# Optimization experiments

Hardware: AMD Instinct MI355X
Metric: run time of the kernel (lower is better)

Reference implementation:

```python
import jax, jax.numpy as jnp
import numpy as np

N = 30000
E = 480000
C_IN, H = 16, 4
NEG_SLOPE = 0.2  # PyG GATv2Conv default negative_slope


def gatv2(x, src, dst, Wl, bl, Wr, br, att, bias, heads, outc, concat, n):
    # PyG GATv2Conv (share_weights=False): e_ij = att . leaky_relu(Wl x_j + Wr x_i)
    xl = (x @ Wl + bl).reshape(n, heads, outc)   # source transform
    xr = (x @ Wr + br).reshape(n, heads, outc)   # target transform
    e = jax.nn.leaky_relu(xl[src] + xr[dst], NEG_SLOPE)        # [E,H,C]
    logits = jnp.einsum('ehc,hc->eh', e, att)                  # [E,H]
    m = jax.lax.stop_gradient(jax.ops.segment_max(logits, dst, num_segments=n))
    ex = jnp.exp(logits - m[dst])
    denom = jax.ops.segment_sum(ex, dst, num_segments=n)
    alpha = ex / denom[dst]                                    # scatter-softmax over in-edges
    out = jax.ops.segment_sum(alpha[:, :, None] * xl[src], dst, num_segments=n)  # [N,H,C]
    out = out.reshape(n, heads * outc) if concat else out.mean(axis=1)
    return out + bias


def setup_inputs() -> dict:
    key = jax.random.key(0)
    ks = jax.random.split(key, 16)
    s = 0.05
    inp = {
        'x': jax.random.uniform(ks[0], (N, C_IN), dtype=jnp.float32),
        'edge_index': jax.random.randint(ks[1], (2, E), 0, N, dtype=jnp.int32),
        'lower_bound': jnp.zeros((C_IN,), jnp.float32),
        'upper_bound': jnp.ones((C_IN,), jnp.float32),
        # Layer 1: GATv2Conv(16 -> 32 per head, heads=4, concat=True) => 128
        'W1l': jax.random.normal(ks[2], (C_IN, H * 32), jnp.float32) * s,
        'b1l': jnp.zeros((H * 32,), jnp.float32),
        'W1r': jax.random.normal(ks[3], (C_IN, H * 32), jnp.float32) * s,
        'b1r': jnp.zeros((H * 32,), jnp.float32),
        'att1': jax.random.normal(ks[4], (H, 32), jnp.float32) * s,
        'bias1': jnp.zeros((H * 32,), jnp.float32),
        # Layer 2: GATv2Conv(128 -> 64 per head, heads=4, concat=False) => 64
        'W2l': jax.random.normal(ks[5], (128, H * 64), jnp.float32) * s,
        'b2l': jnp.zeros((H * 64,), jnp.float32),
        'W2r': jax.random.normal(ks[6], (128, H * 64), jnp.float32) * s,
        'b2r': jnp.zeros((H * 64,), jnp.float32),
        'att2': jax.random.normal(ks[7], (H, 64), jnp.float32) * s,
        'bias2': jnp.zeros((64,), jnp.float32),
        # Final linear head 64 -> 5
        'W3': jax.random.normal(ks[8], (64, 5), jnp.float32) * s,
        'b3': jnp.zeros((5,), jnp.float32),
    }
    return inp


def reference(x, edge_index, lower_bound, upper_bound,
              W1l, b1l, W1r, b1r, att1, bias1,
              W2l, b2l, W2r, b2r, att2, bias2,
              W3, b3):
    n = x.shape[0]
    # min-max normalization
    y = (x - lower_bound) / (upper_bound - lower_bound)
    # add self loops (PyG GATv2Conv default add_self_loops=True)
    loops = jnp.tile(jnp.arange(n, dtype=edge_index.dtype)[None, :], (2, 1))
    ei = jnp.concatenate([edge_index, loops], axis=1)
    src, dst = ei[0], ei[1]
    y = gatv2(y, src, dst, W1l, b1l, W1r, b1r, att1, bias1, H, 32, True, n)
    y = jax.nn.relu(y)
    y = gatv2(y, src, dst, W2l, b2l, W2r, b2r, att2, bias2, H, 64, False, n)
    y = jax.nn.relu(y)
    y = y @ W3 + b3
    return jax.nn.sigmoid(y)
```

## Files before the change

kernel.cpp:

```cpp
#include <hip/hip_runtime.h>

#define H 4
#define D1 128
#define D2 256
#define CIN 16
#define SLOPE 0.2f
#define LOG2E 1.4426950408889634f

typedef short short8v __attribute__((ext_vector_type(8)));
typedef float float4v __attribute__((ext_vector_type(4)));
typedef float float2v __attribute__((ext_vector_type(2)));
typedef __fp16 half2v __attribute__((ext_vector_type(2)));

__device__ __forceinline__ unsigned short f2bf(float f) {
    unsigned int u = __float_as_uint(f);
    u += 0x7FFFu + ((u >> 16) & 1u);
    return (unsigned short)(u >> 16);
}
__device__ __forceinline__ half2v pkrtz(float a, float b) {
    return __builtin_amdgcn_cvt_pkrtz(a, b);
}
__device__ __forceinline__ half2v h2_from_u32(unsigned u) {
    return __builtin_bit_cast(half2v, u);
}
__device__ __forceinline__ unsigned u32_from_h2(half2v h) {
    return __builtin_bit_cast(unsigned, h);
}
__device__ __forceinline__ unsigned short f2fp8x2(float a, float b) {
    return (unsigned short)__builtin_amdgcn_cvt_pk_fp8_f32(a, b, 0, false);
}
template<bool HI>
__device__ __forceinline__ half2v fp8x2_to_h2(unsigned u) {
#if __has_builtin(__builtin_amdgcn_cvt_scalef32_pk_f16_fp8)
    return __builtin_amdgcn_cvt_scalef32_pk_f16_fp8(u, 1.f, HI);
#else
    float2v f = __builtin_amdgcn_cvt_pk_f32_fp8(u, HI);
    return pkrtz(f.x, f.y);
#endif
}
__device__ __forceinline__ float fdot2(half2v a, half2v b, float c) {
#if __has_builtin(__builtin_amdgcn_fdot2)
    return __builtin_amdgcn_fdot2(a, b, c, false);
#else
    return c + (float)a.x * (float)b.x + (float)a.y * (float)b.y;
#endif
}
__device__ __forceinline__ int rfl(int v) {
    return __builtin_amdgcn_readfirstlane(v);
}

__device__ __forceinline__ float dpp_sum16(float x) {
    float t;
    t = __int_as_float(__builtin_amdgcn_mov_dpp(__float_as_int(x), 0xB1, 0xF, 0xF, true));
    x += t;
    t = __int_as_float(__builtin_amdgcn_mov_dpp(__float_as_int(x), 0x4E, 0xF, 0xF, true));
    x += t;
    t = __int_as_float(__builtin_amdgcn_mov_dpp(__float_as_int(x), 0x141, 0xF, 0xF, true));
    x += t;
    t = __int_as_float(__builtin_amdgcn_mov_dpp(__float_as_int(x), 0x140, 0xF, 0xF, true));
    x += t;
    return x;
}

__global__ void k_hist(const int* __restrict__ ei, int E, int ET,
                       int* __restrict__ deg) {
    int idx = blockIdx.x * blockDim.x + threadIdx.x;
    if (idx >= ET) return;
    int dst = (idx < E) ? ei[E + idx] : idx - E;
    atomicAdd(&deg[dst], 1);
}

__global__ __launch_bounds__(1024) void k_scan_one(
        const int* __restrict__ deg, int* __restrict__ rp,
        int* __restrict__ cur, int* __restrict__ ord, int n) {
    __shared__ int wsum[16];
    __shared__ int dh[256];
    int t = threadIdx.x;
    int lane = t & 63, w = t >> 6;
    if (t < 256) dh[t] = 0;
    int base = t * 32;
    int vals[32];
    const int4* dp = (const int4*)deg;
#pragma unroll
    for (int q = 0; q < 8; ++q) {
        int4 v = dp[(base >> 2) + q];
        vals[4 * q + 0] = v.x; vals[4 * q + 1] = v.y;
        vals[4 * q + 2] = v.z; vals[4 * q + 3] = v.w;
    }
    int loc[32];
    int s = 0;
#pragma unroll
    for (int k = 0; k < 32; ++k) {
        int idx = base + k;
        int v = (idx < n) ? vals[k] : 0;
        loc[k] = s;
        s += v;
    }
    int inc = s;
#pragma unroll
    for (int off = 1; off < 64; off <<= 1) {
        int u = __shfl_up(inc, off, 64);
        if (lane >= off) inc += u;
    }
    int excl = inc - s;
    if (lane == 63) wsum[w] = inc;
    __syncthreads();
    if (w == 0) {
        int v = (lane < 16) ? wsum[lane] : 0;
        int winc = v;
#pragma unroll
        for (int off = 1; off < 16; off <<= 1) {
            int u = __shfl_up(winc, off, 64);
            if (lane >= off) winc += u;
        }
        if (lane < 16) wsum[lane] = winc - v;
    }
    __syncthreads();
    int offw = wsum[w] + excl;
#pragma unroll
    for (int q = 0; q < 8; ++q) {
        int i0 = base + 4 * q;
        if (i0 + 3 < n) {
            *(int4*)(rp + i0) = make_int4(offw + loc[4 * q + 0], offw + loc[4 * q + 1],
                                          offw + loc[4 * q + 2], offw + loc[4 * q + 3]);
            *(int4*)(cur + i0) = make_int4(0, 0, 0, 0);
        } else {
#pragma unroll
            for (int e = 0; e < 4; ++e) {
                int idx = i0 + e;
                if (idx < n) { rp[idx] = offw + loc[4 * q + e]; cur[idx] = 0; }
            }
        }
    }
#pragma unroll
    for (int k = 0; k < 32; ++k) {
        int idx = base + k;
        if (idx < n) {
            int bin = 255 - min(vals[k], 255);
            atomicAdd(&dh[bin], 1);
        }
    }
    __syncthreads();
    if (t < 64) {
        int b0 = dh[4 * t], b1 = dh[4 * t + 1], b2 = dh[4 * t + 2], b3 = dh[4 * t + 3];
        int s4 = b0 + b1 + b2 + b3;
        int inc2 = s4;
#pragma unroll
        for (int off = 1; off < 64; off <<= 1) {
            int u = __shfl_up(inc2, off, 64);
            if (lane >= off) inc2 += u;
        }
        int ex = inc2 - s4;
        dh[4 * t] = ex; dh[4 * t + 1] = ex + b0;
        dh[4 * t + 2] = ex + b0 + b1; dh[4 * t + 3] = ex + b0 + b1 + b2;
    }
    __syncthreads();
#pragma unroll
    for (int k = 0; k < 32; ++k) {
        int idx = base + k;
        if (idx < n) {
            int bin = 255 - min(vals[k], 255);
            int pos = atomicAdd(&dh[bin], 1);
            ord[pos] = idx;
        }
    }
}

__global__ void k_fill(const int* __restrict__ ei, int E, int ET,
                       const int* __restrict__ rp, int* __restrict__ cur,
                       int* __restrict__ eord) {
    int idx = blockIdx.x * blockDim.x + threadIdx.x;
    if (idx >= ET) return;
    int src, dst;
    if (idx < E) { src = ei[idx]; dst = ei[E + idx]; }
    else         { src = dst = idx - E; }
    int pos = atomicAdd(&cur[dst], 1);
    eord[rp[dst] + pos] = src;
}

__global__ __launch_bounds__(256) void k_prep(
        const float* __restrict__ x, const float* __restrict__ lb,
        const float* __restrict__ ub,
        const float* __restrict__ Wl, const float* __restrict__ bl,
        const float* __restrict__ Wr, const float* __restrict__ br,
        unsigned char* __restrict__ xl8, unsigned short* __restrict__ xr16,
        const float* __restrict__ W2l, const float* __restrict__ W2r,
        unsigned short* __restrict__ W2t,
        int* __restrict__ deg, int n, int B1) {
    __shared__ float Wls[CIN][D1];
    __shared__ float Wrs[CIN][D1];
    __shared__ float ys[16][CIN];
    int b = blockIdx.x;
    int t = threadIdx.x;
    if (b >= B1) {
        int rb = b - B1;
        if (rb < 256) {
            int idx = rb * 256 + t;
            int k = idx >> 9, c = idx & 511;
            float v = (c < 256) ? W2l[k * 256 + c] : W2r[k * 256 + (c - 256)];
            W2t[(size_t)c * 128 + k] = f2bf(v);
        } else {
            int idx = (rb - 256) * 256 + t;
            if (idx < n) deg[idx] = 0;
        }
        return;
    }
    int i0 = b * 16;
#pragma unroll
    for (int i = 0; i < 8; ++i) {
        int flat = t + 256 * i;
        int k = flat >> 7, c = flat & 127;
        Wls[k][c] = Wl[k * D1 + c];
        Wrs[k][c] = Wr[k * D1 + c];
    }
    {
        int node = t >> 4, k = t & 15;
        int gi = i0 + node;
        float xv = (gi < n) ? x[(size_t)gi * CIN + k] : 0.f;
        ys[node][k] = (xv - lb[k]) / (ub[k] - lb[k]);
    }
    __syncthreads();
    int c = t & 127;
    bool left = t < 128;
    const float (*Ws)[D1] = left ? Wls : Wrs;
    float bias = left ? bl[c] : br[c];
    for (int j = 0; j < 16; ++j) {
        float acc = bias;
#pragma unroll
        for (int k = 0; k < CIN; ++k) acc += ys[j][k] * Ws[k][c];
        int gi = i0 + j;
        float other = __shfl_xor(acc, 1);
        if (gi < n && !(c & 1)) {
            if (left)
                *(unsigned short*)(xl8 + (size_t)gi * D1 + c) = f2fp8x2(acc, other);
            else
                *(unsigned*)(xr16 + (size_t)gi * D1 + c) = u32_from_h2(pkrtz(acc, other));
        }
    }
}

__global__ __launch_bounds__(256) void k_lin2_mfma(
        const unsigned short* __restrict__ h1b,
        const unsigned short* __restrict__ W2t,
        const float* __restrict__ b2l, const float* __restrict__ b2r,
        unsigned char* __restrict__ xl2,
        unsigned short* __restrict__ xr2,
        int n) {
    __shared__ unsigned short At[128 * 128];
    __shared__ unsigned short Bt[128 * 128];
    int t = threadIdx.x;
    int row0 = blockIdx.x * 128;
    int col0 = blockIdx.y * 128;

    {
        int r = t >> 1, hh = (t & 1) * 64;
        bool ok = (row0 + r) < n;
        const unsigned short* gA = h1b + (size_t)(row0 + r) * 128 + hh;
        const unsigned short* gB = W2t + (size_t)(col0 + r) * 128 + hh;
#pragma unroll
        for (int i = 0; i < 8; ++i) {
            uint4 vA = ok ? *(const uint4*)(gA + i * 8) : make_uint4(0, 0, 0, 0);
            uint4 vB = *(const uint4*)(gB + i * 8);
            int col = hh + i * 8;
            int idx = (r * 128 + col) ^ ((r & 15) << 3);
            *(uint4*)&At[idx] = vA;
            *(uint4*)&Bt[idx] = vB;
        }
    }
    __syncthreads();

    int w = t >> 6, l = t & 63;
    int wr = w >> 1, wc = w & 1;
    float4v acc[4][4];
#pragma unroll
    for (int m = 0; m < 4; ++m)
#pragma unroll
        for (int nn = 0; nn < 4; ++nn) acc[m][nn] = (float4v)0.f;

#pragma unroll
    for (int ks = 0; ks < 4; ++ks) {
        int kb = ks * 32 + ((l >> 4) << 3);
        short8v a[4], b[4];
#pragma unroll
        for (int m = 0; m < 4; ++m) {
            int r = wr * 64 + m * 16 + (l & 15);
            a[m] = *(const short8v*)&At[(r * 128 + kb) ^ ((r & 15) << 3)];
        }
#pragma unroll
        for (int nn = 0; nn < 4; ++nn) {
            int c = wc * 64 + nn * 16 + (l & 15);
            b[nn] = *(const short8v*)&Bt[(c * 128 + kb) ^ ((c & 15) << 3)];
        }
#pragma unroll
        for (int m = 0; m < 4; ++m)
#pragma unroll
            for (int nn = 0; nn < 4; ++nn)
                acc[m][nn] = __builtin_amdgcn_mfma_f32_16x16x32_bf16(
                    a[m], b[nn], acc[m][nn], 0, 0, 0);
    }

    if (col0 < 256) {
        const float* bp = b2l;
        int cb = col0;
#pragma unroll
        for (int nn = 0; nn < 4; ++nn) {
            int colc = cb + wc * 64 + nn * 16 + (l & 15);
            float bv = bp[colc];
#pragma unroll
            for (int m = 0; m < 4; ++m) {
                int rbase = row0 + wr * 64 + m * 16 + ((l >> 4) << 2);
#pragma unroll
                for (int r = 0; r < 4; ++r) {
                    int row = rbase + r;
                    float val = acc[m][nn][r] + bv;
                    float other = __shfl_xor(val, 1);
                    if (!(l & 1) && row < n)
                        *(unsigned short*)(xl2 + (size_t)row * 256 + colc) =
                            f2fp8x2(val, other);
                }
            }
        }
    } else {
        const float* bp = b2r;
        int cb = col0 - 256;
#pragma unroll
        for (int nn = 0; nn < 4; ++nn) {
            int colc = cb + wc * 64 + nn * 16 + (l & 15);
            float bv = bp[colc];
#pragma unroll
            for (int m = 0; m < 4; ++m) {
                int rbase = row0 + wr * 64 + m * 16 + ((l >> 4) << 2);
#pragma unroll
                for (int r = 0; r < 4; ++r) {
                    int row = rbase + r;
                    float val = acc[m][nn][r] + bv;
                    float other = __shfl_xor(val, 1);
                    if (!(l & 1) && row < n)
                        *(unsigned*)(xr2 + (size_t)row * 256 + colc) =
                            u32_from_h2(pkrtz(val, other));
                }
            }
        }
    }
}

__global__ __launch_bounds__(256) void k_agg1(
        const unsigned char* __restrict__ xl8, const unsigned short* __restrict__ xr16,
        const float* __restrict__ att, const float* __restrict__ bias,
        const int* __restrict__ rp, const int* __restrict__ deg,
        const int* __restrict__ eord, const int* __restrict__ ord,
        unsigned short* __restrict__ h1b, int n) {
    int t = threadIdx.x;
    int node0 = blockIdx.x * 4 + (t >> 6);
    int l = t & 63;
    bool valid = node0 < n;
    int node = rfl(ord[valid ? node0 : n - 1]);
    half2v xr01 = h2_from_u32(((const unsigned*)xr16)[(size_t)node * 64 + l]);
    float2 av = *(const float2*)(att + 2 * l);
    half2v av01 = pkrtz(av.x * LOG2E, av.y * LOG2E);
    half2v slp = pkrtz(SLOPE, SLOPE);
    int start = rfl(rp[node]);
    int cnt   = valid ? deg[node] : 0;
    cnt = rfl(cnt);
    const unsigned short* xlp = (const unsigned short*)xl8;
    float d = 0.f;
    half2v a01 = pkrtz(0.f, 0.f);
    int cnt4 = cnt & ~3;
    unsigned g0, g1, g2, g3;
    int s0, s1, s2, s3;
    if (cnt4 > 0) {
        int4 iv = *(const int4*)(eord + start);
        s0 = rfl(iv.x); s1 = rfl(iv.y); s2 = rfl(iv.z); s3 = rfl(iv.w);
        g0 = xlp[(unsigned)(s0 << 6) + l]; g1 = xlp[(unsigned)(s1 << 6) + l];
        g2 = xlp[(unsigned)(s2 << 6) + l]; g3 = xlp[(unsigned)(s3 << 6) + l];
    }
    for (int j = 0; j < cnt4; j += 4) {
        unsigned c0 = g0, c1 = g1, c2 = g2, c3 = g3;
        int jn = j + 4;
        if (jn < cnt4) {
            int4 iv = *(const int4*)(eord + start + jn);
            s0 = rfl(iv.x); s1 = rfl(iv.y); s2 = rfl(iv.z); s3 = rfl(iv.w);
            g0 = xlp[(unsigned)(s0 << 6) + l]; g1 = xlp[(unsigned)(s1 << 6) + l];
            g2 = xlp[(unsigned)(s2 << 6) + l]; g3 = xlp[(unsigned)(s3 << 6) + l];
        }
        half2v x0 = fp8x2_to_h2<false>(c0), x1 = fp8x2_to_h2<false>(c1);
        half2v x2 = fp8x2_to_h2<false>(c2), x3 = fp8x2_to_h2<false>(c3);
        half2v s;
        float lg0, lg1, lg2, lg3;
        s = x0 + xr01; s = __builtin_elementwise_max(s, s * slp); lg0 = fdot2(av01, s, 0.f);
        s = x1 + xr01; s = __builtin_elementwise_max(s, s * slp); lg1 = fdot2(av01, s, 0.f);
        s = x2 + xr01; s = __builtin_elementwise_max(s, s * slp); lg2 = fdot2(av01, s, 0.f);
        s = x3 + xr01; s = __builtin_elementwise_max(s, s * slp); lg3 = fdot2(av01, s, 0.f);
        lg0 = dpp_sum16(lg0); lg1 = dpp_sum16(lg1);
        lg2 = dpp_sum16(lg2); lg3 = dpp_sum16(lg3);
        float e0 = exp2f(lg0), e1 = exp2f(lg1);
        float e2 = exp2f(lg2), e3 = exp2f(lg3);
        d += (e0 + e1) + (e2 + e3);
        a01 += pkrtz(e0, e0) * x0;
        a01 += pkrtz(e1, e1) * x1;
        a01 += pkrtz(e2, e2) * x2;
        a01 += pkrtz(e3, e3) * x3;
    }
    for (int j = cnt4; j < cnt; ++j) {
        int sj = rfl(eord[start + j]);
        half2v x0 = fp8x2_to_h2<false>((unsigned)xlp[(unsigned)(sj << 6) + l]);
        half2v s0v = x0 + xr01;
        s0v = __builtin_elementwise_max(s0v, s0v * slp);
        float lg0 = fdot2(av01, s0v, 0.f);
        lg0 = dpp_sum16(lg0);
        float e0 = exp2f(lg0);
        d += e0;
        a01 += pkrtz(e0, e0) * x0;
    }
    if (valid) {
        float inv = 1.f / d;
        float o0 = fmaxf((float)a01.x * inv + bias[2 * l + 0], 0.f);
        float o1 = fmaxf((float)a01.y * inv + bias[2 * l + 1], 0.f);
        ((unsigned*)h1b)[(size_t)node * 64 + l] =
            ((unsigned)f2bf(o1) << 16) | f2bf(o0);
    }
}

__global__ __launch_bounds__(256) void k_agg2(
        const unsigned char* __restrict__ xl8, const unsigned short* __restrict__ xr16,
        const float* __restrict__ att, const float* __restrict__ b2,
        const float* __restrict__ W3, const float* __restrict__ b3,
        const int* __restrict__ rp, const int* __restrict__ deg,
        const int* __restrict__ eord, const int* __restrict__ ord,
        float* __restrict__ out, int n) {
    int t = threadIdx.x;
    int node0 = blockIdx.x * 4 + (t >> 6);
    int l = t & 63;
    bool valid = node0 < n;
    int node = rfl(ord[valid ? node0 : n - 1]);
    uint2 xru = ((const uint2*)xr16)[(size_t)node * 64 + l];
    half2v xr01 = h2_from_u32(xru.x), xr23 = h2_from_u32(xru.y);
    float4 av = *(const float4*)(att + 4 * l);
    half2v av01 = pkrtz(av.x * LOG2E, av.y * LOG2E);
    half2v av23 = pkrtz(av.z * LOG2E, av.w * LOG2E);
    half2v slp = pkrtz(SLOPE, SLOPE);
    int start = rfl(rp[node]);
    int cnt   = valid ? deg[node] : 0;
    cnt = rfl(cnt);
    const unsigned* xlp = (const unsigned*)xl8;
    float d = 0.f;
    half2v a01 = pkrtz(0.f, 0.f), a23 = pkrtz(0.f, 0.f);
    int cnt4 = cnt & ~3;
    unsigned g0, g1, g2, g3;
    int s0, s1, s2, s3;
    if (cnt4 > 0) {
        int4 iv = *(const int4*)(eord + start);
        s0 = rfl(iv.x); s1 = rfl(iv.y); s2 = rfl(iv.z); s3 = rfl(iv.w);
        g0 = xlp[(unsigned)(s0 << 6) + l]; g1 = xlp[(unsigned)(s1 << 6) + l];
        g2 = xlp[(unsigned)(s2 << 6) + l]; g3 = xlp[(unsigned)(s3 << 6) + l];
    }
    for (int j = 0; j < cnt4; j += 4) {
        unsigned c0 = g0, c1 = g1, c2 = g2, c3 = g3;
        int jn = j + 4;
        if (jn < cnt4) {
            int4 iv = *(const int4*)(eord + start + jn);
            s0 = rfl(iv.x); s1 = rfl(iv.y); s2 = rfl(iv.z); s3 = rfl(iv.w);
            g0 = xlp[(unsigned)(s0 << 6) + l]; g1 = xlp[(unsigned)(s1 << 6) + l];
            g2 = xlp[(unsigned)(s2 << 6) + l]; g3 = xlp[(unsigned)(s3 << 6) + l];
        }
        half2v x0lo = fp8x2_to_h2<false>(c0), x0hi = fp8x2_to_h2<true>(c0);
        half2v x1lo = fp8x2_to_h2<false>(c1), x1hi = fp8x2_to_h2<true>(c1);
        half2v x2lo = fp8x2_to_h2<false>(c2), x2hi = fp8x2_to_h2<true>(c2);
        half2v x3lo = fp8x2_to_h2<false>(c3), x3hi = fp8x2_to_h2<true>(c3);
        half2v s;
        float lg0, lg1, lg2, lg3;
        s = x0lo + xr01; s = __builtin_elementwise_max(s, s * slp); lg0 = fdot2(av01, s, 0.f);
        s = x0hi + xr23; s = __builtin_elementwise_max(s, s * slp); lg0 = fdot2(av23, s, lg0);
        s = x1lo + xr01; s = __builtin_elementwise_max(s, s * slp); lg1 = fdot2(av01, s, 0.f);
        s = x1hi + xr23; s = __builtin_elementwise_max(s, s * slp); lg1 = fdot2(av23, s, lg1);
        s = x2lo + xr01; s = __builtin_elementwise_max(s, s * slp); lg2 = fdot2(av01, s, 0.f);
        s = x2hi + xr23; s = __builtin_elementwise_max(s, s * slp); lg2 = fdot2(av23, s, lg2);
        s = x3lo + xr01; s = __builtin_elementwise_max(s, s * slp); lg3 = fdot2(av01, s, 0.f);
        s = x3hi + xr23; s = __builtin_elementwise_max(s, s * slp); lg3 = fdot2(av23, s, lg3);
        lg0 = dpp_sum16(lg0); lg1 = dpp_sum16(lg1);
        lg2 = dpp_sum16(lg2); lg3 = dpp_sum16(lg3);
        float e0 = exp2f(lg0), e1 = exp2f(lg1);
        float e2 = exp2f(lg2), e3 = exp2f(lg3);
        d += (e0 + e1) + (e2 + e3);
        half2v ep;
        ep = pkrtz(e0, e0); a01 += ep * x0lo; a23 += ep * x0hi;
        ep = pkrtz(e1, e1); a01 += ep * x1lo; a23 += ep * x1hi;
        ep = pkrtz(e2, e2); a01 += ep * x2lo; a23 += ep * x2hi;
        ep = pkrtz(e3, e3); a01 += ep * x3lo; a23 += ep * x3hi;
    }
    for (int j = cnt4; j < cnt; ++j) {
        int sj = rfl(eord[start + j]);
        unsigned p0 = xlp[(unsigned)(sj << 6) + l];
        half2v xlo = fp8x2_to_h2<false>(p0), xhi = fp8x2_to_h2<true>(p0);
        half2v s;
        float lg0;
        s = xlo + xr01; s = __builtin_elementwise_max(s, s * slp); lg0 = fdot2(av01, s, 0.f);
        s = xhi + xr23; s = __builtin_elementwise_max(s, s * slp); lg0 = fdot2(av23, s, lg0);
        lg0 = dpp_sum16(lg0);
        float e0 = exp2f(lg0);
        d += e0;
        half2v ep = pkrtz(e0, e0);
        a01 += ep * xlo; a23 += ep * xhi;
    }
    float inv = 1.f / d;
    float v0 = (float)a01.x * inv, v1 = (float)a01.y * inv;
    float v2 = (float)a23.x * inv, v3 = (float)a23.y * inv;
    v0 += __shfl_xor(v0, 16); v1 += __shfl_xor(v1, 16);
    v2 += __shfl_xor(v2, 16); v3 += __shfl_xor(v3, 16);
    v0 += __shfl_xor(v0, 32); v1 += __shfl_xor(v1, 32);
    v2 += __shfl_xor(v2, 32); v3 += __shfl_xor(v3, 32);
    int c0i = 4 * (l & 15);
    v0 = fmaxf(0.25f * v0 + b2[c0i + 0], 0.f);
    v1 = fmaxf(0.25f * v1 + b2[c0i + 1], 0.f);
    v2 = fmaxf(0.25f * v2 + b2[c0i + 2], 0.f);
    v3 = fmaxf(0.25f * v3 + b2[c0i + 3], 0.f);
    float p0, p1, p2, p3, p4;
    {
        const float* w0 = W3 + (c0i + 0) * 5;
        const float* w1 = W3 + (c0i + 1) * 5;
        const float* w2 = W3 + (c0i + 2) * 5;
        const float* w3 = W3 + (c0i + 3) * 5;
        p0 = v0 * w0[0] + v1 * w1[0] + v2 * w2[0] + v3 * w3[0];
        p1 = v0 * w0[1] + v1 * w1[1] + v2 * w2[1] + v3 * w3[1];
        p2 = v0 * w0[2] + v1 * w1[2] + v2 * w2[2] + v3 * w3[2];
        p3 = v0 * w0[3] + v1 * w1[3] + v2 * w2[3] + v3 * w3[3];
        p4 = v0 * w0[4] + v1 * w1[4] + v2 * w2[4] + v3 * w3[4];
    }
    p0 = dpp_sum16(p0); p1 = dpp_sum16(p1); p2 = dpp_sum16(p2);
    p3 = dpp_sum16(p3); p4 = dpp_sum16(p4);
    if (l == 0 && valid) {
        float* o = out + (size_t)node * 5;
        o[0] = 1.f / (1.f + __expf(-(p0 + b3[0])));
        o[1] = 1.f / (1.f + __expf(-(p1 + b3[1])));
        o[2] = 1.f / (1.f + __expf(-(p2 + b3[2])));
        o[3] = 1.f / (1.f + __expf(-(p3 + b3[3])));
        o[4] = 1.f / (1.f + __expf(-(p4 + b3[4])));
    }
}

extern "C" void kernel_launch(void* const* d_in, const int* in_sizes, int n_in,
                              void* d_out, int out_size, void* d_ws, size_t ws_size,
                              hipStream_t stream) {
    const float* x     = (const float*)d_in[0];
    const int*   ei    = (const int*)d_in[1];
    const float* lb    = (const float*)d_in[2];
    const float* ub    = (const float*)d_in[3];
    const float* W1l   = (const float*)d_in[4];
    const float* b1l   = (const float*)d_in[5];
    const float* W1r   = (const float*)d_in[6];
    const float* b1r   = (const float*)d_in[7];
    const float* att1  = (const float*)d_in[8];
    const float* bias1 = (const float*)d_in[9];
    const float* W2l   = (const float*)d_in[10];
    const float* b2l   = (const float*)d_in[11];
    const float* W2r   = (const float*)d_in[12];
    const float* b2r   = (const float*)d_in[13];
    const float* att2  = (const float*)d_in[14];
    const float* bias2 = (const float*)d_in[15];
    const float* W3    = (const float*)d_in[16];
    const float* b3    = (const float*)d_in[17];

    int n  = in_sizes[0] / CIN;
    int E  = in_sizes[1] / 2;
    int ET = E + n;

    char* ws = (char*)d_ws;
    size_t off = 0;
    auto alloc = [&](size_t nbytes) {
        void* p = ws + off;
        off += (nbytes + 255) & ~(size_t)255;
        return p;
    };
    unsigned char*  xl1 = (unsigned char*)alloc((size_t)n * D1);
    unsigned short* xr1 = (unsigned short*)alloc((size_t)n * D1 * 2);
    unsigned short* h1b = (unsigned short*)alloc((size_t)n * D1 * 2);
    unsigned char*  xl2 = (unsigned char*)alloc((size_t)n * D2);
    unsigned short* xr2 = (unsigned short*)alloc((size_t)n * D2 * 2);
    unsigned short* W2t = (unsigned short*)alloc((size_t)512 * 128 * 2);
    int* deg  = (int*)alloc((size_t)n * 4 + 8192);
    int* cur  = (int*)alloc((size_t)n * 4);
    int* rp   = (int*)alloc((size_t)n * 4);
    int* ord  = (int*)alloc((size_t)n * 4);
    int* eord = (int*)alloc((size_t)ET * 4 + 256);

    int B1 = (n + 15) / 16;
    int BZ = (n + 255) / 256;
    k_prep<<<B1 + 256 + BZ, 256, 0, stream>>>(
        x, lb, ub, W1l, b1l, W1r, b1r, xl1, xr1, W2l, W2r, W2t, deg, n, B1);

    k_hist<<<(ET + 255) / 256, 256, 0, stream>>>(ei, E, ET, deg);
    k_scan_one<<<1, 1024, 0, stream>>>(deg, rp, cur, ord, n);
    k_fill<<<(ET + 255) / 256, 256, 0, stream>>>(ei, E, ET, rp, cur, eord);

    k_agg1<<<(n + 3) / 4, 256, 0, stream>>>(xl1, xr1, att1, bias1, rp, deg,
                                            eord, ord, h1b, n);

    dim3 g2((n + 127) / 128, 4);
    k_lin2_mfma<<<g2, 256, 0, stream>>>(h1b, W2t, b2l, b2r, xl2, xr2, n);
    k_agg2<<<(n + 3) / 4, 256, 0, stream>>>(xl2, xr2, att2, bias2, W3, b3,
                                            rp, deg, eord, ord, (float*)d_out, n);
}
```

Baseline: 170.5 us.

## Process four edges per wave concurrently with 16 lanes per edge row

Both aggregation kernels now assign each 16-lane group of a wave to a different edge, so every lane loads a wide vector of the fp8 source row instead of a 2 or 4 byte slice. The per-edge logit reduction shrinks to a 4-lane DPP sum, which matches per-head grouping. Partial accumulators are combined across the four groups with xor shuffles at the end. Remainder edges are handled by masking instead of a scalar tail loop. This aims to cut the number of loop iterations and cross-lane reductions per edge, at the cost of divergent per-lane gather addresses, extra end-of-loop shuffles, and fp16 accumulation being split and re-summed.

```diff
diff --git a/kernel.cpp b/kernel.cpp
--- a/kernel.cpp
+++ b/kernel.cpp
@@ -48,18 +48,19 @@
 __device__ __forceinline__ int rfl(int v) {
     return __builtin_amdgcn_readfirstlane(v);
 }
-
-__device__ __forceinline__ float dpp_sum16(float x) {
+__device__ __forceinline__ float dpp_sum4(float x) {
     float t;
     t = __int_as_float(__builtin_amdgcn_mov_dpp(__float_as_int(x), 0xB1, 0xF, 0xF, true));
     x += t;
     t = __int_as_float(__builtin_amdgcn_mov_dpp(__float_as_int(x), 0x4E, 0xF, 0xF, true));
     x += t;
-    t = __int_as_float(__builtin_amdgcn_mov_dpp(__float_as_int(x), 0x141, 0xF, 0xF, true));
-    x += t;
-    t = __int_as_float(__builtin_amdgcn_mov_dpp(__float_as_int(x), 0x140, 0xF, 0xF, true));
-    x += t;
     return x;
+}
+template<int XOR>
+__device__ __forceinline__ half2v h2_xor_add(half2v v) {
+    unsigned u = u32_from_h2(v);
+    unsigned o = (unsigned)__shfl_xor((int)u, XOR);
+    return v + h2_from_u32(o);
 }
 
 __global__ void k_hist(const int* __restrict__ ei, int E, int ET,
@@ -352,72 +353,77 @@
         unsigned short* __restrict__ h1b, int n) {
     int t = threadIdx.x;
     int node0 = blockIdx.x * 4 + (t >> 6);
-    int l = t & 63;
+    int l = t & 63, g = l >> 4, p = l & 15;
     bool valid = node0 < n;
     int node = rfl(ord[valid ? node0 : n - 1]);
-    half2v xr01 = h2_from_u32(((const unsigned*)xr16)[(size_t)node * 64 + l]);
-    float2 av = *(const float2*)(att + 2 * l);
-    half2v av01 = pkrtz(av.x * LOG2E, av.y * LOG2E);
+    uint4 xq = *(const uint4*)(xr16 + (size_t)node * 128 + p * 8);
+    half2v xr0 = h2_from_u32(xq.x), xr1 = h2_from_u32(xq.y);
+    half2v xr2_ = h2_from_u32(xq.z), xr3 = h2_from_u32(xq.w);
+    const float4* avp = (const float4*)(att + p * 8);
+    float4 af0 = avp[0], af1 = avp[1];
+    half2v av0 = pkrtz(af0.x * LOG2E, af0.y * LOG2E);
+    half2v av1 = pkrtz(af0.z * LOG2E, af0.w * LOG2E);
+    half2v av2 = pkrtz(af1.x * LOG2E, af1.y * LOG2E);
+    half2v av3 = pkrtz(af1.z * LOG2E, af1.w * LOG2E);
     half2v slp = pkrtz(SLOPE, SLOPE);
     int start = rfl(rp[node]);
-    int cnt   = valid ? deg[node] : 0;
+    int cnt = valid ? deg[node] : 0;
     cnt = rfl(cnt);
-    const unsigned short* xlp = (const unsigned short*)xl8;
     float d = 0.f;
-    half2v a01 = pkrtz(0.f, 0.f);
-    int cnt4 = cnt & ~3;
-    unsigned g0, g1, g2, g3;
-    int s0, s1, s2, s3;
-    if (cnt4 > 0) {
-        int4 iv = *(const int4*)(eord + start);
-        s0 = rfl(iv.x); s1 = rfl(iv.y); s2 = rfl(iv.z); s3 = rfl(iv.w);
-        g0 = xlp[(unsigned)(s0 << 6) + l]; g1 = xlp[(unsigned)(s1 << 6) + l];
-        g2 = xlp[(unsigned)(s2 << 6) + l]; g3 = xlp[(unsigned)(s3 << 6) + l];
-    }
-    for (int j = 0; j < cnt4; j += 4) {
-        unsigned c0 = g0, c1 = g1, c2 = g2, c3 = g3;
+    half2v a0 = pkrtz(0.f, 0.f), a1 = a0, a2 = a0, a3 = a0;
+    int cntR = (cnt + 3) & ~3;
+    int ecl = cnt - 1;
+    uint2 row;
+    if (cntR > 0) {
+        int src = eord[start + min(g, ecl)];
+        row = *(const uint2*)(xl8 + ((unsigned)src << 7) + p * 8);
+    }
+    for (int j = 0; j < cntR; j += 4) {
+        uint2 cr = row;
+        bool live = (j + g) <= ecl;
         int jn = j + 4;
-        if (jn < cnt4) {
-            int4 iv = *(const int4*)(eord + start + jn);
-            s0 = rfl(iv.x); s1 = rfl(iv.y); s2 = rfl(iv.z); s3 = rfl(iv.w);
-            g0 = xlp[(unsigned)(s0 << 6) + l]; g1 = xlp[(unsigned)(s1 << 6) + l];
-            g2 = xlp[(unsigned)(s2 << 6) + l]; g3 = xlp[(unsigned)(s3 << 6) + l];
-        }
-        half2v x0 = fp8x2_to_h2<false>(c0), x1 = fp8x2_to_h2<false>(c1);
-        half2v x2 = fp8x2_to_h2<false>(c2), x3 = fp8x2_to_h2<false>(c3);
+        if (jn < cntR) {
+            int src = eord[start + min(jn + g, ecl)];
+            row = *(const uint2*)(xl8 + ((unsigned)src << 7) + p * 8);
+        }
+        half2v x0 = fp8x2_to_h2<false>(cr.x), x1 = fp8x2_to_h2<true>(cr.x);
+        half2v x2 = fp8x2_to_h2<false>(cr.y), x3 = fp8x2_to_h2<true>(cr.y);
         half2v s;
-        float lg0, lg1, lg2, lg3;
-        s = x0 + xr01; s = __builtin_elementwise_max(s, s * slp); lg0 = fdot2(av01, s, 0.f);
-        s = x1 + xr01; s = __builtin_elementwise_max(s, s * slp); lg1 = fdot2(av01, s, 0.f);
-        s = x2 + xr01; s = __builtin_elementwise_max(s, s * slp); lg2 = fdot2(av01, s, 0.f);
-        s = x3 + xr01; s = __builtin_elementwise_max(s, s * slp); lg3 = fdot2(av01, s, 0.f);
-        lg0 = dpp_sum16(lg0); lg1 = dpp_sum16(lg1);
-        lg2 = dpp_sum16(lg2); lg3 = dpp_sum16(lg3);
-        float e0 = exp2f(lg0), e1 = exp2f(lg1);
-        float e2 = exp2f(lg2), e3 = exp2f(lg3);
-        d += (e0 + e1) + (e2 + e3);
-        a01 += pkrtz(e0, e0) * x0;
-        a01 += pkrtz(e1, e1) * x1;
-        a01 += pkrtz(e2, e2) * x2;
-        a01 += pkrtz(e3, e3) * x3;
-    }
-    for (int j = cnt4; j < cnt; ++j) {
-        int sj = rfl(eord[start + j]);
-        half2v x0 = fp8x2_to_h2<false>((unsigned)xlp[(unsigned)(sj << 6) + l]);
-        half2v s0v = x0 + xr01;
-        s0v = __builtin_elementwise_max(s0v, s0v * slp);
-        float lg0 = fdot2(av01, s0v, 0.f);
-        lg0 = dpp_sum16(lg0);
-        float e0 = exp2f(lg0);
-        d += e0;
-        a01 += pkrtz(e0, e0) * x0;
-    }
-    if (valid) {
+        float lg = 0.f;
+        s = x0 + xr0;  s = __builtin_elementwise_max(s, s * slp); lg = fdot2(av0, s, lg);
+        s = x1 + xr1;  s = __builtin_elementwise_max(s, s * slp); lg = fdot2(av1, s, lg);
+        s = x2 + xr2_; s = __builtin_elementwise_max(s, s * slp); lg = fdot2(av2, s, lg);
+        s = x3 + xr3;  s = __builtin_elementwise_max(s, s * slp); lg = fdot2(av3, s, lg);
+        lg = dpp_sum4(lg);
+        float e = exp2f(lg);
+        e = live ? e : 0.f;
+        d += e;
+        half2v ep = pkrtz(e, e);
+        a0 += ep * x0; a1 += ep * x1; a2 += ep * x2; a3 += ep * x3;
+    }
+    d += __shfl_xor(d, 16); d += __shfl_xor(d, 32);
+    a0 = h2_xor_add<16>(a0); a0 = h2_xor_add<32>(a0);
+    a1 = h2_xor_add<16>(a1); a1 = h2_xor_add<32>(a1);
+    a2 = h2_xor_add<16>(a2); a2 = h2_xor_add<32>(a2);
+    a3 = h2_xor_add<16>(a3); a3 = h2_xor_add<32>(a3);
+    if (valid && l < 16) {
         float inv = 1.f / d;
-        float o0 = fmaxf((float)a01.x * inv + bias[2 * l + 0], 0.f);
-        float o1 = fmaxf((float)a01.y * inv + bias[2 * l + 1], 0.f);
-        ((unsigned*)h1b)[(size_t)node * 64 + l] =
-            ((unsigned)f2bf(o1) << 16) | f2bf(o0);
+        const float4* bp = (const float4*)(bias + p * 8);
+        float4 b0 = bp[0], b1 = bp[1];
+        float o0 = fmaxf((float)a0.x * inv + b0.x, 0.f);
+        float o1 = fmaxf((float)a0.y * inv + b0.y, 0.f);
+        float o2 = fmaxf((float)a1.x * inv + b0.z, 0.f);
+        float o3 = fmaxf((float)a1.y * inv + b0.w, 0.f);
+        float o4 = fmaxf((float)a2.x * inv + b1.x, 0.f);
+        float o5 = fmaxf((float)a2.y * inv + b1.y, 0.f);
+        float o6 = fmaxf((float)a3.x * inv + b1.z, 0.f);
+        float o7 = fmaxf((float)a3.y * inv + b1.w, 0.f);
+        uint4 o;
+        o.x = ((unsigned)f2bf(o1) << 16) | f2bf(o0);
+        o.y = ((unsigned)f2bf(o3) << 16) | f2bf(o2);
+        o.z = ((unsigned)f2bf(o5) << 16) | f2bf(o4);
+        o.w = ((unsigned)f2bf(o7) << 16) | f2bf(o6);
+        *(uint4*)(h1b + (size_t)node * 128 + p * 8) = o;
     }
 }
 
@@ -430,104 +436,108 @@
         float* __restrict__ out, int n) {
     int t = threadIdx.x;
     int node0 = blockIdx.x * 4 + (t >> 6);
-    int l = t & 63;
+    int l = t & 63, g = l >> 4, p = l & 15;
     bool valid = node0 < n;
     int node = rfl(ord[valid ? node0 : n - 1]);
-    uint2 xru = ((const uint2*)xr16)[(size_t)node * 64 + l];
-    half2v xr01 = h2_from_u32(xru.x), xr23 = h2_from_u32(xru.y);
-    float4 av = *(const float4*)(att + 4 * l);
-    half2v av01 = pkrtz(av.x * LOG2E, av.y * LOG2E);
-    half2v av23 = pkrtz(av.z * LOG2E, av.w * LOG2E);
+    const uint4* xrq = (const uint4*)(xr16 + (size_t)node * 256 + p * 16);
+    uint4 xa = xrq[0], xb = xrq[1];
+    half2v xr0 = h2_from_u32(xa.x), xr1 = h2_from_u32(xa.y);
+    half2v xr2_ = h2_from_u32(xa.z), xr3 = h2_from_u32(xa.w);
+    half2v xr4 = h2_from_u32(xb.x), xr5 = h2_from_u32(xb.y);
+    half2v xr6 = h2_from_u32(xb.z), xr7 = h2_from_u32(xb.w);
+    const float4* avp = (const float4*)(att + p * 16);
+    float4 af0 = avp[0], af1 = avp[1], af2 = avp[2], af3 = avp[3];
+    half2v av0 = pkrtz(af0.x * LOG2E, af0.y * LOG2E);
+    half2v av1 = pkrtz(af0.z * LOG2E, af0.w * LOG2E);
+    half2v av2 = pkrtz(af1.x * LOG2E, af1.y * LOG2E);
+    half2v av3 = pkrtz(af1.z * LOG2E, af1.w * LOG2E);
+    half2v av4 = pkrtz(af2.x * LOG2E, af2.y * LOG2E);
+    half2v av5 = pkrtz(af2.z * LOG2E, af2.w * LOG2E);
+    half2v av6 = pkrtz(af3.x * LOG2E, af3.y * LOG2E);
+    half2v av7 = pkrtz(af3.z * LOG2E, af3.w * LOG2E);
     half2v slp = pkrtz(SLOPE, SLOPE);
     int start = rfl(rp[node]);
-    int cnt   = valid ? deg[node] : 0;
+    int cnt = valid ? deg[node] : 0;
     cnt = rfl(cnt);
-    const unsigned* xlp = (const unsigned*)xl8;
     float d = 0.f;
-    half2v a01 = pkrtz(0.f, 0.f), a23 = pkrtz(0.f, 0.f);
-    int cnt4 = cnt & ~3;
-    unsigned g0, g1, g2, g3;
-    int s0, s1, s2, s3;
-    if (cnt4 > 0) {
-        int4 iv = *(const int4*)(eord + start);
-        s0 = rfl(iv.x); s1 = rfl(iv.y); s2 = rfl(iv.z); s3 = rfl(iv.w);
-        g0 = xlp[(unsigned)(s0 << 6) + l]; g1 = xlp[(unsigned)(s1 << 6) + l];
-        g2 = xlp[(unsigned)(s2 << 6) + l]; g3 = xlp[(unsigned)(s3 << 6) + l];
-    }
-    for (int j = 0; j < cnt4; j += 4) {
-        unsigned c0 = g0, c1 = g1, c2 = g2, c3 = g3;
+    half2v a0 = pkrtz(0.f, 0.f), a1 = a0, a2 = a0, a3 = a0;
+    half2v a4 = a0, a5 = a0, a6 = a0, a7 = a0;
+    int cntR = (cnt + 3) & ~3;
+    int ecl = cnt - 1;
+    uint4 row;
+    if (cntR > 0) {
+        int src = eord[start + min(g, ecl)];
+        row = *(const uint4*)(xl8 + ((unsigned)src << 8) + p * 16);
+    }
+    for (int j = 0; j < cntR; j += 4) {
+        uint4 cr = row;
+        bool live = (j + g) <= ecl;
         int jn = j + 4;
-        if (jn < cnt4) {
-            int4 iv = *(const int4*)(eord + start + jn);
-            s0 = rfl(iv.x); s1 = rfl(iv.y); s2 = rfl(iv.z); s3 = rfl(iv.w);
-            g0 = xlp[(unsigned)(s0 << 6) + l]; g1 = xlp[(unsigned)(s1 << 6) + l];
-            g2 = xlp[(unsigned)(s2 << 6) + l]; g3 = xlp[(unsigned)(s3 << 6) + l];
-        }
-        half2v x0lo = fp8x2_to_h2<false>(c0), x0hi = fp8x2_to_h2<true>(c0);
-        half2v x1lo = fp8x2_to_h2<false>(c1), x1hi = fp8x2_to_h2<true>(c1);
-        half2v x2lo = fp8x2_to_h2<false>(c2), x2hi = fp8x2_to_h2<true>(c2);
-        half2v x3lo = fp8x2_to_h2<false>(c3), x3hi = fp8x2_to_h2<true>(c3);
+        if (jn < cntR) {
+            int src = eord[start + min(jn + g, ecl)];
+            row = *(const uint4*)(xl8 + ((unsigned)src << 8) + p * 16);
+        }
+        half2v x0 = fp8x2_to_h2<false>(cr.x), x1 = fp8x2_to_h2<true>(cr.x);
+        half2v x2 = fp8x2_to_h2<false>(cr.y), x3 = fp8x2_to_h2<true>(cr.y);
+        half2v x4 = fp8x2_to_h2<false>(cr.z), x5 = fp8x2_to_h2<true>(cr.z);
+        half2v x6 = fp8x2_to_h2<false>(cr.w), x7 = fp8x2_to_h2<true>(cr.w);
         half2v s;
-        float lg0, lg1, lg2, lg3;
-        s = x0lo + xr01; s = __builtin_elementwise_max(s, s * slp); lg0 = fdot2(av01, s, 0.f);
-        s = x0hi + xr23; s = __builtin_elementwise_max(s, s * slp); lg0 = fdot2(av23, s, lg0);
-        s = x1lo + xr01; s = __builtin_elementwise_max(s, s * slp); lg1 = fdot2(av01, s, 0.f);
-        s = x1hi + xr23; s = __builtin_elementwise_max(s, s * slp); lg1 = fdot2(av23, s, lg1);
-        s = x2lo + xr01; s = __builtin_elementwise_max(s, s * slp); lg2 = fdot2(av01, s, 0.f);
-        s = x2hi + xr23; s = __builtin_elementwise_max(s, s * slp); lg2 = fdot2(av23, s, lg2);
-        s = x3lo + xr01; s = __builtin_elementwise_max(s, s * slp); lg3 = fdot2(av01, s, 0.f);
-        s = x3hi + xr23; s = __builtin_elementwise_max(s, s * slp); lg3 = fdot2(av23, s, lg3);
-        lg0 = dpp_sum16(lg0); lg1 = dpp_sum16(lg1);
-        lg2 = dpp_sum16(lg2); lg3 = dpp_sum16(lg3);
-        float e0 = exp2f(lg0), e1 = exp2f(lg1);
-        float e2 = exp2f(lg2), e3 = exp2f(lg3);
-        d += (e0 + e1) + (e2 + e3);
-        half2v ep;
-        ep = pkrtz(e0, e0); a01 += ep * x0lo; a23 += ep * x0hi;
-        ep = pkrtz(e1, e1); a01 += ep * x1lo; a23 += ep * x1hi;
-        ep = pkrtz(e2, e2); a01 += ep * x2lo; a23 += ep * x2hi;
-        ep = pkrtz(e3, e3); a01 += ep * x3lo; a23 += ep * x3hi;
-    }
-    for (int j = cnt4; j < cnt; ++j) {
-        int sj = rfl(eord[start + j]);
-        unsigned p0 = xlp[(unsigned)(sj << 6) + l];
-        half2v xlo = fp8x2_to_h2<false>(p0), xhi = fp8x2_to_h2<true>(p0);
-        half2v s;
-        float lg0;
-        s = xlo + xr01; s = __builtin_elementwise_max(s, s * slp); lg0 = fdot2(av01, s, 0.f);
-        s = xhi + xr23; s = __builtin_elementwise_max(s, s * slp); lg0 = fdot2(av23, s, lg0);
-        lg0 = dpp_sum16(lg0);
-        float e0 = exp2f(lg0);
-        d += e0;
-        half2v ep = pkrtz(e0, e0);
-        a01 += ep * xlo; a23 += ep * xhi;
-    }
-    float inv = 1.f / d;
-    float v0 = (float)a01.x * inv, v1 = (float)a01.y * inv;
-    float v2 = (float)a23.x * inv, v3 = (float)a23.y * inv;
-    v0 += __shfl_xor(v0, 16); v1 += __shfl_xor(v1, 16);
-    v2 += __shfl_xor(v2, 16); v3 += __shfl_xor(v3, 16);
-    v0 += __shfl_xor(v0, 32); v1 += __shfl_xor(v1, 32);
-    v2 += __shfl_xor(v2, 32); v3 += __shfl_xor(v3, 32);
-    int c0i = 4 * (l & 15);
-    v0 = fmaxf(0.25f * v0 + b2[c0i + 0], 0.f);
-    v1 = fmaxf(0.25f * v1 + b2[c0i + 1], 0.f);
-    v2 = fmaxf(0.25f * v2 + b2[c0i + 2], 0.f);
-    v3 = fmaxf(0.25f * v3 + b2[c0i + 3], 0.f);
-    float p0, p1, p2, p3, p4;
-    {
-        const float* w0 = W3 + (c0i + 0) * 5;
-        const float* w1 = W3 + (c0i + 1) * 5;
-        const float* w2 = W3 + (c0i + 2) * 5;
-        const float* w3 = W3 + (c0i + 3) * 5;
-        p0 = v0 * w0[0] + v1 * w1[0] + v2 * w2[0] + v3 * w3[0];
-        p1 = v0 * w0[1] + v1 * w1[1] + v2 * w2[1] + v3 * w3[1];
-        p2 = v0 * w0[2] + v1 * w1[2] + v2 * w2[2] + v3 * w3[2];
-        p3 = v0 * w0[3] + v1 * w1[3] + v2 * w2[3] + v3 * w3[3];
-        p4 = v0 * w0[4] + v1 * w1[4] + v2 * w2[4] + v3 * w3[4];
-    }
-    p0 = dpp_sum16(p0); p1 = dpp_sum16(p1); p2 = dpp_sum16(p2);
-    p3 = dpp_sum16(p3); p4 = dpp_sum16(p4);
+        float lg = 0.f;
+        s = x0 + xr0;  s = __builtin_elementwise_max(s, s * slp); lg = fdot2(av0, s, lg);
+        s = x1 + xr1;  s = __builtin_elementwise_max(s, s * slp); lg = fdot2(av1, s, lg);
+        s = x2 + xr2_; s = __builtin_elementwise_max(s, s * slp); lg = fdot2(av2, s, lg);
+        s = x3 + xr3;  s = __builtin_elementwise_max(s, s * slp); lg = fdot2(av3, s, lg);
+        s = x4 + xr4;  s = __builtin_elementwise_max(s, s * slp); lg = fdot2(av4, s, lg);
+        s = x5 + xr5;  s = __builtin_elementwise_max(s, s * slp); lg = fdot2(av5, s, lg);
+        s = x6 + xr6;  s = __builtin_elementwise_max(s, s * slp); lg = fdot2(av6, s, lg);
+        s = x7 + xr7;  s = __builtin_elementwise_max(s, s * slp); lg = fdot2(av7, s, lg);
+        lg = dpp_sum4(lg);
+        float e = exp2f(lg);
+        e = live ? e : 0.f;
+        d += e;
+        half2v ep = pkrtz(e, e);
+        a0 += ep * x0; a1 += ep * x1; a2 += ep * x2; a3 += ep * x3;
+        a4 += ep * x4; a5 += ep * x5; a6 += ep * x6; a7 += ep * x7;
+    }
+    d += __shfl_xor(d, 16); d += __shfl_xor(d, 32);
+    a0 = h2_xor_add<16>(a0); a0 = h2_xor_add<32>(a0);
+    a1 = h2_xor_add<16>(a1); a1 = h2_xor_add<32>(a1);
+    a2 = h2_xor_add<16>(a2); a2 = h2_xor_add<32>(a2);
+    a3 = h2_xor_add<16>(a3); a3 = h2_xor_add<32>(a3);
+    a4 = h2_xor_add<16>(a4); a4 = h2_xor_add<32>(a4);
+    a5 = h2_xor_add<16>(a5); a5 = h2_xor_add<32>(a5);
+    a6 = h2_xor_add<16>(a6); a6 = h2_xor_add<32>(a6);
+    a7 = h2_xor_add<16>(a7); a7 = h2_xor_add<32>(a7);
+    a0 = h2_xor_add<4>(a0); a0 = h2_xor_add<8>(a0);
+    a1 = h2_xor_add<4>(a1); a1 = h2_xor_add<8>(a1);
+    a2 = h2_xor_add<4>(a2); a2 = h2_xor_add<8>(a2);
+    a3 = h2_xor_add<4>(a3); a3 = h2_xor_add<8>(a3);
+    a4 = h2_xor_add<4>(a4); a4 = h2_xor_add<8>(a4);
+    a5 = h2_xor_add<4>(a5); a5 = h2_xor_add<8>(a5);
+    a6 = h2_xor_add<4>(a6); a6 = h2_xor_add<8>(a6);
+    a7 = h2_xor_add<4>(a7); a7 = h2_xor_add<8>(a7);
+    float inv = 0.25f / d;
+    int q4 = p & 3;
+    float m[16];
+    m[0]  = (float)a0.x * inv; m[1]  = (float)a0.y * inv;
+    m[2]  = (float)a1.x * inv; m[3]  = (float)a1.y * inv;
+    m[4]  = (float)a2.x * inv; m[5]  = (float)a2.y * inv;
+    m[6]  = (float)a3.x * inv; m[7]  = (float)a3.y * inv;
+    m[8]  = (float)a4.x * inv; m[9]  = (float)a4.y * inv;
+    m[10] = (float)a5.x * inv; m[11] = (float)a5.y * inv;
+    m[12] = (float)a6.x * inv; m[13] = (float)a6.y * inv;
+    m[14] = (float)a7.x * inv; m[15] = (float)a7.y * inv;
+    int c0 = 16 * q4;
+    float p0 = 0.f, p1 = 0.f, p2 = 0.f, p3 = 0.f, p4 = 0.f;
+#pragma unroll
+    for (int k = 0; k < 16; ++k) {
+        float v = fmaxf(m[k] + b2[c0 + k], 0.f);
+        const float* wrow = W3 + (c0 + k) * 5;
+        p0 += v * wrow[0]; p1 += v * wrow[1]; p2 += v * wrow[2];
+        p3 += v * wrow[3]; p4 += v * wrow[4];
+    }
+    p0 = dpp_sum4(p0); p1 = dpp_sum4(p1); p2 = dpp_sum4(p2);
+    p3 = dpp_sum4(p3); p4 = dpp_sum4(p4);
     if (l == 0 && valid) {
         float* o = out + (size_t)node * 5;
         o[0] = 1.f / (1.f + __expf(-(p0 + b3[0])));
```

New measurement: 195.9 us. 14.9% more time.
